# Optimization experiments

Hardware: AMD Instinct MI355X
Metric: run time of the kernel (lower is better)

## Reference

```python
import jax, jax.numpy as jnp
import numpy as np

EPS = 1e-12
NUM_IDS = 25          # instance ids 0..24 (0 = background)
INTER_MARGIN = 0.2
W_SEM_ALIGN, W_SEM_MEM, W_INS_CON, W_INS_MEM = 0.5, 1.0, 1.0, 1.0


def _l2norm(x, axis):
    return x / jnp.maximum(jnp.linalg.norm(x, axis=axis, keepdims=True), EPS)


def _flat_pix(x):  # [B,T,C,H,W] -> [B*T*H*W, C]
    B, T, C, H, W = x.shape
    return jnp.transpose(x, (0, 1, 3, 4, 2)).reshape(B * T * H * W, C)


def _seg_ids(mask_r):  # [B,T,Hp,Wp] int -> [BT*N] global segment ids
    B, T, Hp, Wp = mask_r.shape
    bt = jnp.arange(B * T, dtype=jnp.int32)[:, None] * NUM_IDS
    return (mask_r.reshape(B * T, Hp * Wp) + bt).reshape(-1)


def _mask_nearest_half(inst_mask):
    # torch nearest interp H -> H/2 picks src index floor(i*2) = 2i
    return inst_mask[:, :, ::2, ::2]


def _gt_bilinear_half(x):
    B, T, C, H, W = x.shape
    return x.reshape(B, T, C, H // 2, 2, W // 2, 2).mean(axis=(4, 6))


def _sem_align_loss(refined_sem, lseg_gt, inst_mask):
    # fused replacement of the per-(b,t,instance) python loops: one segment-reduce pass
    B, T, C, Hp, Wp = refined_sem.shape
    mask_r = _mask_nearest_half(inst_mask)
    gt = _l2norm(_gt_bilinear_half(lseg_gt), axis=2)
    pred = _l2norm(refined_sem, axis=2)
    predf, gtf = _flat_pix(pred), _flat_pix(gt)
    seg = _seg_ids(mask_r)
    nseg = B * T * NUM_IDS
    sums = jax.ops.segment_sum(gtf, seg, num_segments=nseg)
    cnts = jax.ops.segment_sum(jnp.ones_like(seg, jnp.float32), seg, num_segments=nseg)
    # normalize(mean) == normalize(sum); prototype is detached in the original
    proto = jax.lax.stop_gradient(_l2norm(sums, axis=1))
    cos_loss = 1.0 - jnp.sum(predf * proto[seg], axis=1)
    valid = (mask_r.reshape(-1) > 0) & (cnts[seg] >= 2.0)
    total = jnp.sum(jnp.where(valid, cos_loss, 0.0))
    count = jnp.maximum(jnp.sum(valid.astype(jnp.float32)), 1.0)
    return total / count


def _memory_loss(pred_feat, mem_feat, mem_mask):
    pred = _l2norm(pred_feat, axis=2)
    tgt = jax.lax.stop_gradient(_l2norm(mem_feat, axis=2))
    cos_dist = (1.0 - jnp.sum(pred * tgt, axis=2, keepdims=True)) * mem_mask
    return jnp.sum(cos_dist) / jnp.maximum(jnp.sum(mem_mask), 1.0)


def _ins_contrastive_loss(refined_ins, inst_mask):
    # ContrastiveLoss(inter_mode='hinge', inter_margin=0.2, normalize_feats=True)
    B, T, C, Hp, Wp = refined_ins.shape
    mask_r = _mask_nearest_half(inst_mask)
    feat = _l2norm(refined_ins, axis=2)
    featf = _flat_pix(feat)
    seg = _seg_ids(mask_r)
    nseg = B * T * NUM_IDS
    sums = jax.ops.segment_sum(featf, seg, num_segments=nseg)
    cnts = jax.ops.segment_sum(jnp.ones_like(seg, jnp.float32), seg, num_segments=nseg)
    proto = _l2norm(sums, axis=1)  # [BT*K, C]
    # intra: pull pixels toward their instance prototype
    cos_loss = 1.0 - jnp.sum(featf * proto[seg], axis=1)
    valid = (mask_r.reshape(-1) > 0) & (cnts[seg] >= 2.0)
    intra = jnp.sum(jnp.where(valid, cos_loss, 0.0)) / jnp.maximum(
        jnp.sum(valid.astype(jnp.float32)), 1.0)
    # inter: hinge pushing apart prototypes of different instances within a scene
    P = proto.reshape(B * T, NUM_IDS, C)
    vmask = (cnts.reshape(B * T, NUM_IDS) >= 2.0) & (jnp.arange(NUM_IDS)[None, :] > 0)
    sim = jnp.einsum('bkc,blc->bkl', P, P)
    pair = vmask[:, :, None] & vmask[:, None, :] & ~jnp.eye(NUM_IDS, dtype=bool)[None]
    hinge = jnp.maximum(sim - INTER_MARGIN, 0.0)
    inter = jnp.sum(jnp.where(pair, hinge, 0.0)) / jnp.maximum(
        jnp.sum(pair.astype(jnp.float32)), 1.0)
    return intra + inter


def setup_inputs() -> dict:
    key = jax.random.key(0)
    ks = jax.random.split(key, 7)
    B, T, C_SEM, C_INS, HP, WP = 2, 4, 512, 64, 64, 64
    H, W = 2 * HP, 2 * WP
    return {
        "refined_sem": jax.random.normal(ks[0], (B, T, C_SEM, HP, WP), jnp.float32),
        "refined_ins": jax.random.normal(ks[1], (B, T, C_INS, HP, WP), jnp.float32),
        "lseg_gt": jax.random.normal(ks[2], (B, T, C_SEM, H, W), jnp.float32),
        "mem_sem": jax.random.normal(ks[3], (B, T, C_SEM, HP, WP), jnp.float32),
        "mem_ins": jax.random.normal(ks[4], (B, T, C_INS, HP, WP), jnp.float32),
        "mem_mask": (jax.random.uniform(ks[5], (B, T, 1, HP, WP)) < 0.7).astype(jnp.float32),
        "inst_mask": jax.random.randint(ks[6], (B, T, H, W), 0, NUM_IDS, dtype=jnp.int32),
    }


def reference(refined_sem, refined_ins, lseg_gt, mem_sem, mem_ins, mem_mask, inst_mask):
    sem_align = _sem_align_loss(refined_sem, lseg_gt, inst_mask)
    sem_mem = _memory_loss(refined_sem, mem_sem, mem_mask)
    ins_con = _ins_contrastive_loss(refined_ins, inst_mask)
    ins_mem = _memory_loss(refined_ins, mem_ins, mem_mask)
    objective = (W_SEM_ALIGN * sem_align + W_SEM_MEM * sem_mem
                 + W_INS_CON * ins_con + W_INS_MEM * ins_mem)
    return objective
```

## Files before the change

kernel.cpp:

```cpp
#include <hip/hip_runtime.h>

typedef unsigned short u16;
typedef unsigned int u32;
typedef unsigned long long u64;

#define NID 25


#define SC16  65536.0f
#define ISC16 (1.0f/65536.0f)
#define SC20  1048576.0f
#define ISC20 (1.0f/1048576.0f)
#define SC32  4294967296.0f

__device__ __forceinline__ float bf2f(u16 h){ return __uint_as_float(((u32)h) << 16); }
__device__ __forceinline__ u16 f2bf(float f){
  u32 u = __float_as_uint(f);
  u32 r = u + 0x7fffu + ((u >> 16) & 1u);
  return (u16)(r >> 16);
}

template<bool BF>
__device__ __forceinline__ float LD(const void* p, size_t i){
  if constexpr (BF) return bf2f(((const u16*)p)[i]);
  else return ((const float*)p)[i];
}
template<bool BF>
__device__ __forceinline__ float2 LD2(const void* p, size_t i){
  if constexpr (BF){
    ushort2 v = *(const ushort2*)((const u16*)p + i);
    return make_float2(bf2f(v.x), bf2f(v.y));
  } else {
    return *(const float2*)((const float*)p + i);
  }
}
template<bool BF>
__device__ __forceinline__ float4 LD4(const void* p, size_t i){
  if constexpr (BF){
    ushort4 v = *(const ushort4*)((const u16*)p + i);
    return make_float4(bf2f(v.x), bf2f(v.y), bf2f(v.z), bf2f(v.w));
  } else {
    return *(const float4*)((const float*)p + i);
  }
}

__global__ __launch_bounds__(256) void k_probe(const u32* __restrict__ x,
                                               int* __restrict__ flag){
  __shared__ int cnt;
  if (threadIdx.x == 0) cnt = 0;
  __syncthreads();
  int c = 0;
  for (int i = threadIdx.x; i < 1024; i += 256){
    u32 e = (x[i] >> 7) & 0xffu;
    c += (e >= 100 && e <= 140) ? 1 : 0;
  }
  atomicAdd(&cnt, c);
  __syncthreads();
  if (threadIdx.x == 0) *flag = (cnt >= 600) ? 1 : 0;
}

template<bool BF>
__device__ void p1a_body(const void* lg, int* __restrict__ ss){
  __shared__ int ps[64];
  const int t = threadIdx.x;
  const int hr = blockIdx.x;
  const int cg = blockIdx.y;
  const int bt = blockIdx.z;
  const int q2 = t & 31;
  const int cw = t >> 5;
  if (t < 64) ps[t] = 0;
  __syncthreads();
  float s0 = 0.f, s1 = 0.f;
  const int c0 = cg*64 + cw*8;
  #pragma unroll
  for (int k = 0; k < 8; ++k){
    const size_t o = ((size_t)(bt*512 + c0 + k) << 14) + (hr << 8) + (q2 << 2);
    float4 a = LD4<BF>(lg, o);
    float4 b = LD4<BF>(lg, o + 128);
    const float m0 = (a.x + a.y + b.x + b.y) * 0.25f;
    const float m1 = (a.z + a.w + b.z + b.w) * 0.25f;
    s0 += m0*m0; s1 += m1*m1;
  }
  atomicAdd(&ps[q2*2],     (int)rintf(s0 * SC20));
  atomicAdd(&ps[q2*2 + 1], (int)rintf(s1 * SC20));
  __syncthreads();
  if (t < 64){
    const int v = ps[t];
    if (v) atomicAdd(&ss[(bt << 12) + (hr << 6) + t], v);
  }
}
__global__ __launch_bounds__(256) void k_p1a(const void* lg, int* ss,
                                             const int* flag){
  if (*flag) p1a_body<true>(lg, ss);
  else       p1a_body<false>(lg, ss);
}

template<bool BF>
__device__ void p1b_body(const void* lg, const int* __restrict__ im,
                         const int* __restrict__ ss,
                         int* __restrict__ sem_sums, int* __restrict__ cnts){
  __shared__ int sums[4*25*129];
  __shared__ float invl[128];
  __shared__ int hist[NID];
  const int t = threadIdx.x;
  const int bt = blockIdx.y;
  const int pxb = blockIdx.x * 128;
  const int q = t & 127;
  const int cw = t >> 7;
  for (int k = t; k < 4*25*129; k += 512) sums[k] = 0;
  if (t < NID) hist[t] = 0;
  const int p = pxb + q;
  const int id = im[(bt << 14) + ((p >> 6) << 8) + ((p & 63) << 1)];
  if (t < 128){
    const float sf = (float)ss[(bt << 12) + pxb + t] * ISC20;
    invl[t] = SC16 / fmaxf(sqrtf(sf), 1e-12f);
  }
  __syncthreads();
  if (t < 128) atomicAdd(&hist[id], 1);
  const float inv = invl[q];
  const size_t pbase = ((size_t)(bt*512 + cw*128) << 14)
                     + ((p >> 6) << 8) + ((p & 63) << 1);
  int* dst = &sums[(cw*25 + id)*129];
  #pragma unroll 8
  for (int k = 0; k < 128; ++k){
    const size_t o = pbase + ((size_t)k << 14);
    float2 a = LD2<BF>(lg, o);
    float2 b = LD2<BF>(lg, o + 128);
    const float m = (a.x + a.y + b.x + b.y) * 0.25f;
    atomicAdd(&dst[k], (int)rintf(m * inv));
  }
  __syncthreads();
  for (int k = t; k < 25*512; k += 512){
    const int id2 = k >> 9, c2 = k & 511, cw2 = c2 >> 7, k2 = c2 & 127;
    const int v = sums[(cw2*25 + id2)*129 + k2];
    if (v) atomicAdd(&sem_sums[(bt*NID + id2)*512 + c2], v);
  }
  if (t < NID && hist[t] > 0) atomicAdd(&cnts[bt*NID + t], hist[t]);
}
__global__ __launch_bounds__(512) void k_p1b(const void* lg, const int* im,
    const int* ss, int* sem_sums, int* cnts, const int* flag){
  if (*flag) p1b_body<true>(lg, im, ss, sem_sums, cnts);
  else       p1b_body<false>(lg, im, ss, sem_sums, cnts);
}

template<bool BF>
__device__ void p4_body(const void* ri, const int* __restrict__ im,
                        int* __restrict__ ins_sums){
  __shared__ int   sums[2*25*33];
  __shared__ float parts[2][128];
  const int t = threadIdx.x;
  const int pb = blockIdx.x * 128;
  const int bt = pb >> 12;
  const int h = t >> 7, q = t & 127;
  const int p = (pb + q) & 4095;
  const int id = im[(bt << 14) + ((p >> 6) << 8) + ((p & 63) << 1)];
  for (int k = t; k < 2*25*33; k += 256) sums[k] = 0;
  float vals[32];
  float ffh = 0.f;
  #pragma unroll
  for (int cc = 0; cc < 32; ++cc){
    float v = LD<BF>(ri, (size_t)(bt*64 + h*32 + cc)*4096 + p);
    vals[cc] = v; ffh += v*v;
  }
  parts[h][q] = ffh;
  __syncthreads();
  const float inv = SC16 / fmaxf(sqrtf(parts[0][q] + parts[1][q]), 1e-12f);
  int* dst = &sums[h*825 + id*33];
  #pragma unroll
  for (int cc = 0; cc < 32; ++cc) atomicAdd(&dst[cc], (int)rintf(vals[cc]*inv));
  __syncthreads();
  for (int k = t; k < 1600; k += 256){
    const int id2 = k >> 6, c2 = k & 63, h2 = c2 >> 5, cc2 = c2 & 31;
    const int v = sums[h2*825 + id2*33 + cc2];
    if (v) atomicAdd(&ins_sums[(bt*NID + id2)*64 + c2], v);
  }
}
__global__ __launch_bounds__(256) void k_p4(const void* ri, const int* im,
    int* ins_sums, const int* flag){
  if (*flag) p4_body<true>(ri, im, ins_sums);
  else       p4_body<false>(ri, im, ins_sums);
}

__global__ __launch_bounds__(256) void k_p5(const int* __restrict__ sem_sums,
    const int* __restrict__ ins_sums, const int* __restrict__ cnts,
    float* __restrict__ proto_sem, float* __restrict__ proto_ins,
    int* __restrict__ valid_tab){
  const int wg = blockIdx.x*4 + (threadIdx.x >> 6);
  const int l  = threadIdx.x & 63;
  if (blockIdx.x < 50){
    const int seg = wg;
    float v[8]; float ss = 0.f;
    const size_t base = (size_t)seg*512 + l;
    #pragma unroll
    for (int k = 0; k < 8; ++k){
      v[k] = (float)sem_sums[base + 64*k] * ISC16;
      ss += v[k]*v[k];
    }
    for (int m = 1; m < 64; m <<= 1) ss += __shfl_xor(ss, m, 64);
    const float inv = 1.f / fmaxf(sqrtf(ss), 1e-12f);
    #pragma unroll
    for (int k = 0; k < 8; ++k) proto_sem[base + 64*k] = v[k]*inv;
    if (l == 0) valid_tab[seg] = (cnts[seg] >= 2 && (seg % NID) != 0) ? 1 : 0;
  } else {
    const int seg = wg - 200;
    float v = (float)ins_sums[(size_t)seg*64 + l] * ISC16;
    float ss = v*v;
    for (int m = 1; m < 64; m <<= 1) ss += __shfl_xor(ss, m, 64);
    proto_ins[(size_t)seg*64 + l] = v * (1.f / fmaxf(sqrtf(ss), 1e-12f));
  }
}

template<bool BF>
__device__ void p3_body(const void* rs, const void* ms, const void* mmask,
    const int* __restrict__ im, const float* __restrict__ proto_sem,
    const int* __restrict__ valid_tab, u64* __restrict__ sc){
  __shared__ float protoT[25*513];
  __shared__ float4 parts[8][64];
  __shared__ int vt[NID];
  const int t = threadIdx.x;
  const int pb = blockIdx.x * 64;
  const int bt = pb >> 12;
  const int w  = t >> 5;
  const int l2 = t & 31;
  for (int f = t; f < 12800; f += 256){
    const int id2 = f >> 9, c2 = f & 511;
    protoT[id2*513 + c2] = proto_sem[(size_t)(bt*NID + id2)*512 + c2];
  }
  if (t < NID) vt[t] = valid_tab[bt*NID + t];
  __syncthreads();
  const int p0 = (pb & 4095) + 2*l2;
  const int p1 = p0 + 1;
  const int id0 = im[(bt << 14) + ((p0 >> 6) << 8) + ((p0 & 63) << 1)];
  const int id1 = im[(bt << 14) + ((p1 >> 6) << 8) + ((p1 & 63) << 1)];
  const size_t cbase = (size_t)(bt*512 + w*64)*4096 + p0;
  const float* pr0 = &protoT[id0*513 + w*64];
  const float* pr1 = &protoT[id1*513 + w*64];
  float pp0=0.f,pp1=0.f,pm0=0.f,pm1=0.f,mm0=0.f,mm1=0.f,pd0=0.f,pd1=0.f;
  #pragma unroll 8
  for (int cc = 0; cc < 64; ++cc){
    float2 pv = LD2<BF>(rs, cbase + (size_t)cc*4096);
    float2 mv = LD2<BF>(ms, cbase + (size_t)cc*4096);
    pp0 += pv.x*pv.x; pp1 += pv.y*pv.y;
    mm0 += mv.x*mv.x; mm1 += mv.y*mv.y;
    pm0 += pv.x*mv.x; pm1 += pv.y*mv.y;
    pd0 += pv.x*pr0[cc]; pd1 += pv.y*pr1[cc];
  }
  parts[w][2*l2]   = make_float4(pp0, pm0, mm0, pd0);
  parts[w][2*l2+1] = make_float4(pp1, pm1, mm1, pd1);
  __syncthreads();
  if (t < 64){
    float ppn=0.f, pm=0.f, mm=0.f, pd=0.f;
    #pragma unroll
    for (int k = 0; k < 8; ++k){
      float4 f4 = parts[k][t];
      ppn += f4.x; pm += f4.y; mm += f4.z; pd += f4.w;
    }
    const int g = pb + t;
    const int p = g & 4095;
    const int id = im[(bt << 14) + ((p >> 6) << 8) + ((p & 63) << 1)];
    const float npn = fmaxf(sqrtf(ppn), 1e-12f);
    const int vld = vt[id];
    float a_i = vld ? (1.f - pd/npn) : 0.f;
    float vc  = vld ? 1.f : 0.f;
    float mkv = LD<BF>(mmask, g);
    const float nmn = fmaxf(sqrtf(mm), 1e-12f);
    float s_i = mkv * (1.f - pm/(npn*nmn));
    for (int m = 1; m < 64; m <<= 1){
      a_i += __shfl_xor(a_i, m, 64);
      vc  += __shfl_xor(vc,  m, 64);
      s_i += __shfl_xor(s_i, m, 64);
      mkv += __shfl_xor(mkv, m, 64);
    }
    if (t == 0){
      long long v0 = llrintf(a_i * SC32);
      long long v2 = llrintf(s_i * SC32);
      if (v0) atomicAdd(&sc[0], (u64)v0);
      if (vc != 0.f) atomicAdd(&sc[1], (u64)llrintf(vc));
      if (v2) atomicAdd(&sc[2], (u64)v2);
      if (mkv != 0.f) atomicAdd(&sc[3], (u64)llrintf(mkv));
    }
  }
}
__global__ __launch_bounds__(256) void k_p3(const void* rs, const void* ms,
    const void* mmask, const int* im, const float* proto_sem,
    const int* valid_tab, u64* sc, const int* flag){
  if (*flag) p3_body<true>(rs, ms, mmask, im, proto_sem, valid_tab, sc);
  else       p3_body<false>(rs, ms, mmask, im, proto_sem, valid_tab, sc);
}

template<bool BF>
__device__ void p6_body(const void* ri, const void* mi, const void* mmask,
    const int* __restrict__ im, const float* __restrict__ proto_ins,
    const int* __restrict__ valid_tab, u64* __restrict__ sc){
  __shared__ float protoT[25*65];
  __shared__ float4 parts[4][128];
  __shared__ int vt[NID];
  const int t = threadIdx.x;
  const int pb = blockIdx.x * 128;
  const int bt = pb >> 12;
  const int h2 = t >> 6;
  const int q2 = t & 63;
  for (int f = t; f < 1600; f += 256){
    const int id2 = f >> 6, c2 = f & 63;
    protoT[id2*65 + c2] = proto_ins[(size_t)(bt*NID + id2)*64 + c2];
  }
  if (t < NID) vt[t] = valid_tab[bt*NID + t];
  __syncthreads();
  const int p0 = (pb & 4095) + 2*q2;
  const int p1 = p0 + 1;
  const int id0 = im[(bt << 14) + ((p0 >> 6) << 8) + ((p0 & 63) << 1)];
  const int id1 = im[(bt << 14) + ((p1 >> 6) << 8) + ((p1 & 63) << 1)];
  const size_t cbase = (size_t)(bt*64 + h2*16)*4096 + p0;
  const float* pr0 = &protoT[id0*65 + h2*16];
  const float* pr1 = &protoT[id1*65 + h2*16];
  float ff0=0.f,ff1=0.f,fm0=0.f,fm1=0.f,m20=0.f,m21=0.f,fd0=0.f,fd1=0.f;
  #pragma unroll
  for (int cc = 0; cc < 16; ++cc){
    float2 fv = LD2<BF>(ri, cbase + (size_t)cc*4096);
    float2 mv = LD2<BF>(mi, cbase + (size_t)cc*4096);
    ff0 += fv.x*fv.x; ff1 += fv.y*fv.y;
    m20 += mv.x*mv.x; m21 += mv.y*mv.y;
    fm0 += fv.x*mv.x; fm1 += fv.y*mv.y;
    fd0 += fv.x*pr0[cc]; fd1 += fv.y*pr1[cc];
  }
  parts[h2][2*q2]   = make_float4(ff0, fm0, m20, fd0);
  parts[h2][2*q2+1] = make_float4(ff1, fm1, m21, fd1);
  __syncthreads();
  if (t < 128){
    float ff=0.f, fm=0.f, m2=0.f, fd=0.f;
    #pragma unroll
    for (int k = 0; k < 4; ++k){
      float4 f4 = parts[k][t];
      ff += f4.x; fm += f4.y; m2 += f4.z; fd += f4.w;
    }
    const int g = pb + t;
    const int p = g & 4095;
    const int id = im[(bt << 14) + ((p >> 6) << 8) + ((p & 63) << 1)];
    const float nf = fmaxf(sqrtf(ff), 1e-12f);
    float ii = vt[id] ? (1.f - fd/nf) : 0.f;
    const float mkv = LD<BF>(mmask, g);
    const float nm = fmaxf(sqrtf(m2), 1e-12f);
    float mi_ = mkv * (1.f - fm/(nf*nm));
    for (int m = 1; m < 64; m <<= 1){
      ii  += __shfl_xor(ii,  m, 64);
      mi_ += __shfl_xor(mi_, m, 64);
    }
    if ((t & 63) == 0){
      long long v4 = llrintf(ii  * SC32);
      long long v5 = llrintf(mi_ * SC32);
      if (v4) atomicAdd(&sc[4], (u64)v4);
      if (v5) atomicAdd(&sc[5], (u64)v5);
    }
  }
}
__global__ __launch_bounds__(256) void k_p6(const void* ri, const void* mi,
    const void* mmask, const int* im, const float* proto_ins,
    const int* valid_tab, u64* sc, const int* flag){
  if (*flag) p6_body<true>(ri, mi, mmask, im, proto_ins, valid_tab, sc);
  else       p6_body<false>(ri, mi, mmask, im, proto_ins, valid_tab, sc);
}

__global__ __launch_bounds__(256) void k_f(const float* __restrict__ proto_ins,
    const int* __restrict__ valid_tab, const u64* __restrict__ sc,
    u32* __restrict__ out){
  __shared__ float P[25*65];
  __shared__ int vt[NID];
  __shared__ float red[8];
  const int t = threadIdx.x;
  float hsum = 0.f, pcnt = 0.f;
  for (int bt = 0; bt < 8; ++bt){
    __syncthreads();
    for (int f = t; f < 1600; f += 256){
      const int id2 = f >> 6, c2 = f & 63;
      P[id2*65 + c2] = proto_ins[bt*1600 + f];
    }
    if (t < NID) vt[t] = valid_tab[bt*NID + t];
    __syncthreads();
    for (int kl = t; kl < 625; kl += 256){
      const int k = kl / 25, l = kl - k*25;
      if (k != l && vt[k] && vt[l]){
        float s = 0.f;
        #pragma unroll
        for (int c = 0; c < 64; ++c) s += P[k*65 + c] * P[l*65 + c];
        hsum += fmaxf(s - 0.2f, 0.f);
        pcnt += 1.f;
      }
    }
  }
  for (int m = 1; m < 64; m <<= 1){
    hsum += __shfl_xor(hsum, m, 64);
    pcnt += __shfl_xor(pcnt, m, 64);
  }
  __syncthreads();
  if ((t & 63) == 0){ red[t >> 6] = hsum; red[4 + (t >> 6)] = pcnt; }
  __syncthreads();
  if (t == 0){
    const float inter = red[0]+red[1]+red[2]+red[3];
    const float pc    = red[4]+red[5]+red[6]+red[7];
    const double S = 1.0 / 4294967296.0;
    const double asum = (double)(long long)sc[0] * S;
    const double vcnt = (double)(long long)sc[1];
    const double ssum = (double)(long long)sc[2] * S;
    const double mcnt = (double)(long long)sc[3];
    const double isum = (double)(long long)sc[4] * S;
    const double msum = (double)(long long)sc[5] * S;
    const double align = asum / (vcnt > 1.0 ? vcnt : 1.0);
    const double smem  = ssum / (mcnt > 1.0 ? mcnt : 1.0);
    const double intra = isum / (vcnt > 1.0 ? vcnt : 1.0);
    const double imem  = msum / (mcnt > 1.0 ? mcnt : 1.0);
    const double obj = 0.5*align + smem + intra + (double)(inter / fmaxf(pc, 1.f)) + imem;
    const u32 b = (u32)f2bf((float)obj);
    out[0] = (b << 16) | b;
  }
}

extern "C" void kernel_launch(void* const* d_in, const int* in_sizes, int n_in,
                              void* d_out, int out_size, void* d_ws, size_t ws_size,
                              hipStream_t stream){
  const void* rs    = d_in[0];
  const void* ri    = d_in[1];
  const void* lg    = d_in[2];
  const void* ms    = d_in[3];
  const void* mi    = d_in[4];
  const void* mmask = d_in[5];
  const int*  im    = (const int*)d_in[6];

  char* ws = (char*)d_ws;
  u64*   sc        = (u64*)  ws;
  int*   flag      = (int*)  (ws + 64);
  int*   cnts      = (int*)  (ws + 256);
  int*   sem_sums  = (int*)  (ws + 4096);
  int*   ins_sums  = (int*)  (ws + 413696);
  int*   ss        = (int*)  (ws + 466944);
  float* proto_sem = (float*)(ws + 466944);
  float* proto_ins = (float*)(ws + 876544);
  int*   valid_tab = (int*)  (ws + 927744);

  hipMemsetAsync(d_ws, 0, 598016, stream);
  k_probe<<<1, 256, 0, stream>>>((const u32*)rs, flag);
  k_p1a<<<dim3(64, 8, 8), 256, 0, stream>>>(lg, ss, flag);
  k_p1b<<<dim3(32, 8), 512, 0, stream>>>(lg, im, ss, sem_sums, cnts, flag);
  k_p4<<<256, 256, 0, stream>>>(ri, im, ins_sums, flag);
  k_p5<<<100, 256, 0, stream>>>(sem_sums, ins_sums, cnts, proto_sem, proto_ins, valid_tab);
  k_p3<<<512, 256, 0, stream>>>(rs, ms, mmask, im, proto_sem, valid_tab, sc, flag);
  k_p6<<<256, 256, 0, stream>>>(ri, mi, mmask, im, proto_ins, valid_tab, sc, flag);
  k_f<<<1, 256, 0, stream>>>(proto_ins, valid_tab, sc, (u32*)d_out);
}
```

Baseline: 579.3 us.

## Fuse instance sums into p1a launch and merge loss tail kernels

Folds the instance prototype accumulation into the p1a grid as an extra z-slice. It also merges the semantic/instance cosine passes and the inter-instance hinge into one tail kernel, with a trivial finalize kernel. The tail blocks now read prototypes straight from global memory instead of staging the full table in LDS. They also use smaller pixel tiles and wave shuffles for partial reductions. This aims to cut launch count, LDS staging and occupancy limits, at the cost of uncoalesced prototype reads from cache.

```diff
diff --git a/kernel.cpp b/kernel.cpp
--- a/kernel.cpp
+++ b/kernel.cpp
@@ -89,10 +89,54 @@
     if (v) atomicAdd(&ss[(bt << 12) + (hr << 6) + t], v);
   }
 }
-__global__ __launch_bounds__(256) void k_p1a(const void* lg, int* ss,
-                                             const int* flag){
-  if (*flag) p1a_body<true>(lg, ss);
-  else       p1a_body<false>(lg, ss);
+
+template<bool BF>
+__device__ void p4_body(const void* ri, const int* __restrict__ im,
+                        int* __restrict__ ins_sums, int qb){
+  __shared__ int   sums[2*25*33];
+  __shared__ float parts[2][128];
+  const int t = threadIdx.x;
+  const int pb = qb * 128;
+  const int bt = pb >> 12;
+  const int h = t >> 7, q = t & 127;
+  const int p = (pb + q) & 4095;
+  const int id = im[(bt << 14) + ((p >> 6) << 8) + ((p & 63) << 1)];
+  for (int k = t; k < 2*25*33; k += 256) sums[k] = 0;
+  float vals[32];
+  float ffh = 0.f;
+  #pragma unroll
+  for (int cc = 0; cc < 32; ++cc){
+    float v = LD<BF>(ri, (size_t)(bt*64 + h*32 + cc)*4096 + p);
+    vals[cc] = v; ffh += v*v;
+  }
+  parts[h][q] = ffh;
+  __syncthreads();
+  const float inv = SC16 / fmaxf(sqrtf(parts[0][q] + parts[1][q]), 1e-12f);
+  int* dst = &sums[h*825 + id*33];
+  #pragma unroll
+  for (int cc = 0; cc < 32; ++cc) atomicAdd(&dst[cc], (int)rintf(vals[cc]*inv));
+  __syncthreads();
+  for (int k = t; k < 1600; k += 256){
+    const int id2 = k >> 6, c2 = k & 63, h2 = c2 >> 5, cc2 = c2 & 31;
+    const int v = sums[h2*825 + id2*33 + cc2];
+    if (v) atomicAdd(&ins_sums[(bt*NID + id2)*64 + c2], v);
+  }
+}
+
+template<bool BF>
+__device__ void a_body(const void* lg, int* ss, const void* ri,
+                       const int* im, int* ins_sums){
+  if (blockIdx.z < 8){
+    p1a_body<BF>(lg, ss);
+  } else {
+    const int q = blockIdx.y*64 + blockIdx.x;
+    if (q < 256) p4_body<BF>(ri, im, ins_sums, q);
+  }
+}
+__global__ __launch_bounds__(256) void k_a(const void* lg, int* ss,
+    const void* ri, const int* im, int* ins_sums, const int* flag){
+  if (*flag) a_body<true>(lg, ss, ri, im, ins_sums);
+  else       a_body<false>(lg, ss, ri, im, ins_sums);
 }
 
 template<bool BF>
@@ -141,44 +185,6 @@
     const int* ss, int* sem_sums, int* cnts, const int* flag){
   if (*flag) p1b_body<true>(lg, im, ss, sem_sums, cnts);
   else       p1b_body<false>(lg, im, ss, sem_sums, cnts);
-}
-
-template<bool BF>
-__device__ void p4_body(const void* ri, const int* __restrict__ im,
-                        int* __restrict__ ins_sums){
-  __shared__ int   sums[2*25*33];
-  __shared__ float parts[2][128];
-  const int t = threadIdx.x;
-  const int pb = blockIdx.x * 128;
-  const int bt = pb >> 12;
-  const int h = t >> 7, q = t & 127;
-  const int p = (pb + q) & 4095;
-  const int id = im[(bt << 14) + ((p >> 6) << 8) + ((p & 63) << 1)];
-  for (int k = t; k < 2*25*33; k += 256) sums[k] = 0;
-  float vals[32];
-  float ffh = 0.f;
-  #pragma unroll
-  for (int cc = 0; cc < 32; ++cc){
-    float v = LD<BF>(ri, (size_t)(bt*64 + h*32 + cc)*4096 + p);
-    vals[cc] = v; ffh += v*v;
-  }
-  parts[h][q] = ffh;
-  __syncthreads();
-  const float inv = SC16 / fmaxf(sqrtf(parts[0][q] + parts[1][q]), 1e-12f);
-  int* dst = &sums[h*825 + id*33];
-  #pragma unroll
-  for (int cc = 0; cc < 32; ++cc) atomicAdd(&dst[cc], (int)rintf(vals[cc]*inv));
-  __syncthreads();
-  for (int k = t; k < 1600; k += 256){
-    const int id2 = k >> 6, c2 = k & 63, h2 = c2 >> 5, cc2 = c2 & 31;
-    const int v = sums[h2*825 + id2*33 + cc2];
-    if (v) atomicAdd(&ins_sums[(bt*NID + id2)*64 + c2], v);
-  }
-}
-__global__ __launch_bounds__(256) void k_p4(const void* ri, const int* im,
-    int* ins_sums, const int* flag){
-  if (*flag) p4_body<true>(ri, im, ins_sums);
-  else       p4_body<false>(ri, im, ins_sums);
 }
 
 __global__ __launch_bounds__(256) void k_p5(const int* __restrict__ sem_sums,
@@ -211,65 +217,65 @@
 }
 
 template<bool BF>
-__device__ void p3_body(const void* rs, const void* ms, const void* mmask,
+__device__ void p3n_body(const void* rs, const void* ms, const void* mmask,
     const int* __restrict__ im, const float* __restrict__ proto_sem,
-    const int* __restrict__ valid_tab, u64* __restrict__ sc){
-  __shared__ float protoT[25*513];
-  __shared__ float4 parts[8][64];
-  __shared__ int vt[NID];
-  const int t = threadIdx.x;
-  const int pb = blockIdx.x * 64;
+    const int* __restrict__ valid_tab, u64* __restrict__ sc, float4* parts){
+  const int t = threadIdx.x;
+  const int pb = blockIdx.x * 32;
   const int bt = pb >> 12;
-  const int w  = t >> 5;
-  const int l2 = t & 31;
-  for (int f = t; f < 12800; f += 256){
-    const int id2 = f >> 9, c2 = f & 511;
-    protoT[id2*513 + c2] = proto_sem[(size_t)(bt*NID + id2)*512 + c2];
-  }
-  if (t < NID) vt[t] = valid_tab[bt*NID + t];
-  __syncthreads();
-  const int p0 = (pb & 4095) + 2*l2;
-  const int p1 = p0 + 1;
+  const int px0 = pb & 4095;
+  const int w  = t >> 4;
+  const int l2 = t & 15;
+  const int p0 = px0 + 2*l2, p1 = p0 + 1;
   const int id0 = im[(bt << 14) + ((p0 >> 6) << 8) + ((p0 & 63) << 1)];
   const int id1 = im[(bt << 14) + ((p1 >> 6) << 8) + ((p1 & 63) << 1)];
-  const size_t cbase = (size_t)(bt*512 + w*64)*4096 + p0;
-  const float* pr0 = &protoT[id0*513 + w*64];
-  const float* pr1 = &protoT[id1*513 + w*64];
+  const float* __restrict__ pr0 = proto_sem + ((size_t)(bt*NID + id0) << 9) + w*32;
+  const float* __restrict__ pr1 = proto_sem + ((size_t)(bt*NID + id1) << 9) + w*32;
+  const size_t cbase = ((size_t)(bt*512 + w*32) << 12) + p0;
   float pp0=0.f,pp1=0.f,pm0=0.f,pm1=0.f,mm0=0.f,mm1=0.f,pd0=0.f,pd1=0.f;
   #pragma unroll 8
-  for (int cc = 0; cc < 64; ++cc){
-    float2 pv = LD2<BF>(rs, cbase + (size_t)cc*4096);
-    float2 mv = LD2<BF>(ms, cbase + (size_t)cc*4096);
+  for (int cc = 0; cc < 32; ++cc){
+    float2 pv = LD2<BF>(rs, cbase + ((size_t)cc << 12));
+    float2 mv = LD2<BF>(ms, cbase + ((size_t)cc << 12));
     pp0 += pv.x*pv.x; pp1 += pv.y*pv.y;
     mm0 += mv.x*mv.x; mm1 += mv.y*mv.y;
     pm0 += pv.x*mv.x; pm1 += pv.y*mv.y;
     pd0 += pv.x*pr0[cc]; pd1 += pv.y*pr1[cc];
   }
-  parts[w][2*l2]   = make_float4(pp0, pm0, mm0, pd0);
-  parts[w][2*l2+1] = make_float4(pp1, pm1, mm1, pd1);
-  __syncthreads();
-  if (t < 64){
-    float ppn=0.f, pm=0.f, mm=0.f, pd=0.f;
-    #pragma unroll
-    for (int k = 0; k < 8; ++k){
-      float4 f4 = parts[k][t];
-      ppn += f4.x; pm += f4.y; mm += f4.z; pd += f4.w;
-    }
-    const int g = pb + t;
-    const int p = g & 4095;
+  #pragma unroll
+  for (int m = 16; m <= 32; m <<= 1){
+    pp0 += __shfl_xor(pp0, m, 64); pp1 += __shfl_xor(pp1, m, 64);
+    pm0 += __shfl_xor(pm0, m, 64); pm1 += __shfl_xor(pm1, m, 64);
+    mm0 += __shfl_xor(mm0, m, 64); mm1 += __shfl_xor(mm1, m, 64);
+    pd0 += __shfl_xor(pd0, m, 64); pd1 += __shfl_xor(pd1, m, 64);
+  }
+  const int lane = t & 63, wv = t >> 6;
+  if (lane < 16){
+    parts[wv*32 + 2*lane]     = make_float4(pp0, pm0, mm0, pd0);
+    parts[wv*32 + 2*lane + 1] = make_float4(pp1, pm1, mm1, pd1);
+  }
+  __syncthreads();
+  if (t < 32){
+    float4 s0 = parts[t], s1 = parts[32+t], s2 = parts[64+t], s3 = parts[96+t];
+    const float ppn = s0.x+s1.x+s2.x+s3.x;
+    const float pm  = s0.y+s1.y+s2.y+s3.y;
+    const float mm  = s0.z+s1.z+s2.z+s3.z;
+    const float pd  = s0.w+s1.w+s2.w+s3.w;
+    const int p = px0 + t, g = pb + t;
     const int id = im[(bt << 14) + ((p >> 6) << 8) + ((p & 63) << 1)];
+    const int vld = valid_tab[bt*NID + id];
     const float npn = fmaxf(sqrtf(ppn), 1e-12f);
-    const int vld = vt[id];
     float a_i = vld ? (1.f - pd/npn) : 0.f;
     float vc  = vld ? 1.f : 0.f;
     float mkv = LD<BF>(mmask, g);
     const float nmn = fmaxf(sqrtf(mm), 1e-12f);
     float s_i = mkv * (1.f - pm/(npn*nmn));
-    for (int m = 1; m < 64; m <<= 1){
-      a_i += __shfl_xor(a_i, m, 64);
-      vc  += __shfl_xor(vc,  m, 64);
-      s_i += __shfl_xor(s_i, m, 64);
-      mkv += __shfl_xor(mkv, m, 64);
+    #pragma unroll
+    for (int m = 1; m < 32; m <<= 1){
+      a_i += __shfl_xor(a_i, m, 32);
+      vc  += __shfl_xor(vc,  m, 32);
+      s_i += __shfl_xor(s_i, m, 32);
+      mkv += __shfl_xor(mkv, m, 32);
     }
     if (t == 0){
       long long v0 = llrintf(a_i * SC32);
@@ -281,71 +287,64 @@
     }
   }
 }
-__global__ __launch_bounds__(256) void k_p3(const void* rs, const void* ms,
-    const void* mmask, const int* im, const float* proto_sem,
-    const int* valid_tab, u64* sc, const int* flag){
-  if (*flag) p3_body<true>(rs, ms, mmask, im, proto_sem, valid_tab, sc);
-  else       p3_body<false>(rs, ms, mmask, im, proto_sem, valid_tab, sc);
-}
-
-template<bool BF>
-__device__ void p6_body(const void* ri, const void* mi, const void* mmask,
+
+template<bool BF>
+__device__ void p6n_body(const void* ri, const void* mi, const void* mmask,
     const int* __restrict__ im, const float* __restrict__ proto_ins,
-    const int* __restrict__ valid_tab, u64* __restrict__ sc){
-  __shared__ float protoT[25*65];
-  __shared__ float4 parts[4][128];
-  __shared__ int vt[NID];
-  const int t = threadIdx.x;
-  const int pb = blockIdx.x * 128;
+    const int* __restrict__ valid_tab, u64* __restrict__ sc, float4* parts){
+  const int t = threadIdx.x;
+  const int bx = (int)blockIdx.x - 1024;
+  const int pb = bx * 64;
   const int bt = pb >> 12;
-  const int h2 = t >> 6;
-  const int q2 = t & 63;
-  for (int f = t; f < 1600; f += 256){
-    const int id2 = f >> 6, c2 = f & 63;
-    protoT[id2*65 + c2] = proto_ins[(size_t)(bt*NID + id2)*64 + c2];
-  }
-  if (t < NID) vt[t] = valid_tab[bt*NID + t];
-  __syncthreads();
-  const int p0 = (pb & 4095) + 2*q2;
-  const int p1 = p0 + 1;
+  const int px0 = pb & 4095;
+  const int h  = t >> 5;
+  const int l2 = t & 31;
+  const int p0 = px0 + 2*l2, p1 = p0 + 1;
   const int id0 = im[(bt << 14) + ((p0 >> 6) << 8) + ((p0 & 63) << 1)];
   const int id1 = im[(bt << 14) + ((p1 >> 6) << 8) + ((p1 & 63) << 1)];
-  const size_t cbase = (size_t)(bt*64 + h2*16)*4096 + p0;
-  const float* pr0 = &protoT[id0*65 + h2*16];
-  const float* pr1 = &protoT[id1*65 + h2*16];
+  const float* __restrict__ pr0 = proto_ins + (size_t)(bt*NID + id0)*64 + h*8;
+  const float* __restrict__ pr1 = proto_ins + (size_t)(bt*NID + id1)*64 + h*8;
+  const size_t cbase = ((size_t)(bt*64 + h*8) << 12) + p0;
   float ff0=0.f,ff1=0.f,fm0=0.f,fm1=0.f,m20=0.f,m21=0.f,fd0=0.f,fd1=0.f;
   #pragma unroll
-  for (int cc = 0; cc < 16; ++cc){
-    float2 fv = LD2<BF>(ri, cbase + (size_t)cc*4096);
-    float2 mv = LD2<BF>(mi, cbase + (size_t)cc*4096);
+  for (int cc = 0; cc < 8; ++cc){
+    float2 fv = LD2<BF>(ri, cbase + ((size_t)cc << 12));
+    float2 mv = LD2<BF>(mi, cbase + ((size_t)cc << 12));
     ff0 += fv.x*fv.x; ff1 += fv.y*fv.y;
     m20 += mv.x*mv.x; m21 += mv.y*mv.y;
     fm0 += fv.x*mv.x; fm1 += fv.y*mv.y;
     fd0 += fv.x*pr0[cc]; fd1 += fv.y*pr1[cc];
   }
-  parts[h2][2*q2]   = make_float4(ff0, fm0, m20, fd0);
-  parts[h2][2*q2+1] = make_float4(ff1, fm1, m21, fd1);
-  __syncthreads();
-  if (t < 128){
-    float ff=0.f, fm=0.f, m2=0.f, fd=0.f;
-    #pragma unroll
-    for (int k = 0; k < 4; ++k){
-      float4 f4 = parts[k][t];
-      ff += f4.x; fm += f4.y; m2 += f4.z; fd += f4.w;
-    }
-    const int g = pb + t;
-    const int p = g & 4095;
+  ff0 += __shfl_xor(ff0, 32, 64); ff1 += __shfl_xor(ff1, 32, 64);
+  fm0 += __shfl_xor(fm0, 32, 64); fm1 += __shfl_xor(fm1, 32, 64);
+  m20 += __shfl_xor(m20, 32, 64); m21 += __shfl_xor(m21, 32, 64);
+  fd0 += __shfl_xor(fd0, 32, 64); fd1 += __shfl_xor(fd1, 32, 64);
+  const int lane = t & 63, wv = t >> 6;
+  if (lane < 32){
+    parts[wv*64 + 2*lane]     = make_float4(ff0, fm0, m20, fd0);
+    parts[wv*64 + 2*lane + 1] = make_float4(ff1, fm1, m21, fd1);
+  }
+  __syncthreads();
+  if (t < 64){
+    float4 s0 = parts[t], s1 = parts[64+t], s2 = parts[128+t], s3 = parts[192+t];
+    const float ff = s0.x+s1.x+s2.x+s3.x;
+    const float fm = s0.y+s1.y+s2.y+s3.y;
+    const float m2 = s0.z+s1.z+s2.z+s3.z;
+    const float fd = s0.w+s1.w+s2.w+s3.w;
+    const int p = px0 + t, g = pb + t;
     const int id = im[(bt << 14) + ((p >> 6) << 8) + ((p & 63) << 1)];
+    const int vld = valid_tab[bt*NID + id];
     const float nf = fmaxf(sqrtf(ff), 1e-12f);
-    float ii = vt[id] ? (1.f - fd/nf) : 0.f;
-    const float mkv = LD<BF>(mmask, g);
+    float ii = vld ? (1.f - fd/nf) : 0.f;
+    float mkv = LD<BF>(mmask, g);
     const float nm = fmaxf(sqrtf(m2), 1e-12f);
     float mi_ = mkv * (1.f - fm/(nf*nm));
+    #pragma unroll
     for (int m = 1; m < 64; m <<= 1){
       ii  += __shfl_xor(ii,  m, 64);
       mi_ += __shfl_xor(mi_, m, 64);
     }
-    if ((t & 63) == 0){
+    if (t == 0){
       long long v4 = llrintf(ii  * SC32);
       long long v5 = llrintf(mi_ * SC32);
       if (v4) atomicAdd(&sc[4], (u64)v4);
@@ -353,50 +352,71 @@
     }
   }
 }
-__global__ __launch_bounds__(256) void k_p6(const void* ri, const void* mi,
-    const void* mmask, const int* im, const float* proto_ins,
-    const int* valid_tab, u64* sc, const int* flag){
-  if (*flag) p6_body<true>(ri, mi, mmask, im, proto_ins, valid_tab, sc);
-  else       p6_body<false>(ri, mi, mmask, im, proto_ins, valid_tab, sc);
-}
-
-__global__ __launch_bounds__(256) void k_f(const float* __restrict__ proto_ins,
-    const int* __restrict__ valid_tab, const u64* __restrict__ sc,
-    u32* __restrict__ out){
-  __shared__ float P[25*65];
-  __shared__ int vt[NID];
-  __shared__ float red[8];
-  const int t = threadIdx.x;
+
+__device__ void fh_body(const float* __restrict__ proto_ins,
+                        const int* __restrict__ valid_tab, u64* __restrict__ sc,
+                        float* P, int* vt, float* red){
+  const int bt = (int)blockIdx.x - 1536;
+  const int t = threadIdx.x;
+  for (int f = t; f < 1600; f += 256){
+    P[(f >> 6)*65 + (f & 63)] = proto_ins[bt*1600 + f];
+  }
+  if (t < NID) vt[t] = valid_tab[bt*NID + t];
+  __syncthreads();
   float hsum = 0.f, pcnt = 0.f;
-  for (int bt = 0; bt < 8; ++bt){
-    __syncthreads();
-    for (int f = t; f < 1600; f += 256){
-      const int id2 = f >> 6, c2 = f & 63;
-      P[id2*65 + c2] = proto_ins[bt*1600 + f];
-    }
-    if (t < NID) vt[t] = valid_tab[bt*NID + t];
-    __syncthreads();
-    for (int kl = t; kl < 625; kl += 256){
-      const int k = kl / 25, l = kl - k*25;
-      if (k != l && vt[k] && vt[l]){
-        float s = 0.f;
-        #pragma unroll
-        for (int c = 0; c < 64; ++c) s += P[k*65 + c] * P[l*65 + c];
-        hsum += fmaxf(s - 0.2f, 0.f);
-        pcnt += 1.f;
-      }
+  for (int kl = t; kl < 625; kl += 256){
+    const int k = kl / 25, l = kl - k*25;
+    if (k != l && vt[k] && vt[l]){
+      float s = 0.f;
+      #pragma unroll
+      for (int c = 0; c < 64; ++c) s += P[k*65 + c] * P[l*65 + c];
+      hsum += fmaxf(s - 0.2f, 0.f);
+      pcnt += 1.f;
     }
   }
   for (int m = 1; m < 64; m <<= 1){
     hsum += __shfl_xor(hsum, m, 64);
     pcnt += __shfl_xor(pcnt, m, 64);
   }
-  __syncthreads();
   if ((t & 63) == 0){ red[t >> 6] = hsum; red[4 + (t >> 6)] = pcnt; }
   __syncthreads();
   if (t == 0){
-    const float inter = red[0]+red[1]+red[2]+red[3];
-    const float pc    = red[4]+red[5]+red[6]+red[7];
+    const float h  = red[0]+red[1]+red[2]+red[3];
+    const float pc = red[4]+red[5]+red[6]+red[7];
+    long long v6 = llrintf(h * SC32);
+    if (v6) atomicAdd(&sc[6], (u64)v6);
+    if (pc != 0.f) atomicAdd(&sc[7], (u64)llrintf(pc));
+  }
+}
+
+template<bool BF>
+__device__ void tail_body(const void* rs, const void* ms, const void* ri,
+    const void* mi, const void* mmask, const int* im,
+    const float* proto_sem, const float* proto_ins, const int* valid_tab,
+    u64* sc, float4* parts3, float4* parts6, float* P, int* vt, float* red){
+  const u32 bx = blockIdx.x;
+  if (bx < 1024)      p3n_body<BF>(rs, ms, mmask, im, proto_sem, valid_tab, sc, parts3);
+  else if (bx < 1536) p6n_body<BF>(ri, mi, mmask, im, proto_ins, valid_tab, sc, parts6);
+  else                fh_body(proto_ins, valid_tab, sc, P, vt, red);
+}
+__global__ __launch_bounds__(256) void k_tail(const void* rs, const void* ms,
+    const void* ri, const void* mi, const void* mmask, const int* im,
+    const float* proto_sem, const float* proto_ins, const int* valid_tab,
+    u64* sc, const int* flag){
+  __shared__ float4 parts3[128];
+  __shared__ float4 parts6[256];
+  __shared__ float  P[25*65];
+  __shared__ int    vt[NID];
+  __shared__ float  red[8];
+  if (*flag) tail_body<true>(rs, ms, ri, mi, mmask, im, proto_sem, proto_ins,
+                             valid_tab, sc, parts3, parts6, P, vt, red);
+  else       tail_body<false>(rs, ms, ri, mi, mmask, im, proto_sem, proto_ins,
+                              valid_tab, sc, parts3, parts6, P, vt, red);
+}
+
+__global__ __launch_bounds__(64) void k_f2(const u64* __restrict__ sc,
+                                           u32* __restrict__ out){
+  if (threadIdx.x == 0){
     const double S = 1.0 / 4294967296.0;
     const double asum = (double)(long long)sc[0] * S;
     const double vcnt = (double)(long long)sc[1];
@@ -404,11 +424,14 @@
     const double mcnt = (double)(long long)sc[3];
     const double isum = (double)(long long)sc[4] * S;
     const double msum = (double)(long long)sc[5] * S;
+    const double hsum = (double)(long long)sc[6] * S;
+    const double pc   = (double)(long long)sc[7];
     const double align = asum / (vcnt > 1.0 ? vcnt : 1.0);
     const double smem  = ssum / (mcnt > 1.0 ? mcnt : 1.0);
     const double intra = isum / (vcnt > 1.0 ? vcnt : 1.0);
     const double imem  = msum / (mcnt > 1.0 ? mcnt : 1.0);
-    const double obj = 0.5*align + smem + intra + (double)(inter / fmaxf(pc, 1.f)) + imem;
+    const double interv = hsum / (pc > 1.0 ? pc : 1.0);
+    const double obj = 0.5*align + smem + intra + interv + imem;
     const u32 b = (u32)f2bf((float)obj);
     out[0] = (b << 16) | b;
   }
@@ -431,18 +454,17 @@
   int*   cnts      = (int*)  (ws + 256);
   int*   sem_sums  = (int*)  (ws + 4096);
   int*   ins_sums  = (int*)  (ws + 413696);
-  int*   ss        = (int*)  (ws + 466944);
+  int*   ssq       = (int*)  (ws + 466944);
   float* proto_sem = (float*)(ws + 466944);
   float* proto_ins = (float*)(ws + 876544);
   int*   valid_tab = (int*)  (ws + 927744);
 
   hipMemsetAsync(d_ws, 0, 598016, stream);
   k_probe<<<1, 256, 0, stream>>>((const u32*)rs, flag);
-  k_p1a<<<dim3(64, 8, 8), 256, 0, stream>>>(lg, ss, flag);
-  k_p1b<<<dim3(32, 8), 512, 0, stream>>>(lg, im, ss, sem_sums, cnts, flag);
-  k_p4<<<256, 256, 0, stream>>>(ri, im, ins_sums, flag);
+  k_a<<<dim3(64, 8, 9), 256, 0, stream>>>(lg, ssq, ri, im, ins_sums, flag);
+  k_p1b<<<dim3(32, 8), 512, 0, stream>>>(lg, im, ssq, sem_sums, cnts, flag);
   k_p5<<<100, 256, 0, stream>>>(sem_sums, ins_sums, cnts, proto_sem, proto_ins, valid_tab);
-  k_p3<<<512, 256, 0, stream>>>(rs, ms, mmask, im, proto_sem, valid_tab, sc, flag);
-  k_p6<<<256, 256, 0, stream>>>(ri, mi, mmask, im, proto_ins, valid_tab, sc, flag);
-  k_f<<<1, 256, 0, stream>>>(proto_ins, valid_tab, sc, (u32*)d_out);
-}
+  k_tail<<<1544, 256, 0, stream>>>(rs, ms, ri, mi, mmask, im, proto_sem,
+                                   proto_ins, valid_tab, sc, flag);
+  k_f2<<<1, 64, 0, stream>>>(sc, (u32*)d_out);
+}
```

Result: no change. 581.8 us (+0.4%).
